# Kernel optimization log

Hardware: AMD Instinct MI355X
Metric: run time of the kernel (lower is better)

## Reference

```python
import jax, jax.numpy as jnp
import numpy as np

N_NODES = 100_000
N_EDGES = 3_200_000
NUM_FEATURES = 128
HIDDEN = 128
NUM_CLASSES = 10
LAYERS = 3
NUM_GRAPHS = 256
EPS = 1e-5


def setup_inputs() -> dict:
    key = jax.random.key(0)
    ks = jax.random.split(key, 12)
    s = 0.05
    x = jax.random.normal(ks[0], (N_NODES, NUM_FEATURES), jnp.float32)
    edge_index = jax.random.randint(ks[1], (2, N_EDGES), 0, N_NODES, dtype=jnp.int32)
    batch = jnp.sort(jax.random.randint(ks[2], (N_NODES,), 0, NUM_GRAPHS, dtype=jnp.int32))
    lin1_W = jax.random.normal(ks[3], (NUM_FEATURES, HIDDEN), jnp.float32) * s
    lin1_b = jnp.zeros((HIDDEN,), jnp.float32)
    conv_W = jax.random.normal(ks[4], (LAYERS, HIDDEN, HIDDEN), jnp.float32) * s
    conv_b = jnp.zeros((LAYERS, HIDDEN), jnp.float32)
    mlp_W1 = jax.random.normal(ks[5], (HIDDEN, HIDDEN), jnp.float32) * s
    mlp_b1 = jnp.zeros((HIDDEN,), jnp.float32)
    mlp_W2 = jax.random.normal(ks[6], (HIDDEN, NUM_CLASSES), jnp.float32) * s
    mlp_b2 = jnp.zeros((NUM_CLASSES,), jnp.float32)
    return {
        'x': x, 'edge_index': edge_index, 'batch': batch,
        'lin1_W': lin1_W, 'lin1_b': lin1_b,
        'conv_W': conv_W, 'conv_b': conv_b,
        'mlp_W1': mlp_W1, 'mlp_b1': mlp_b1,
        'mlp_W2': mlp_W2, 'mlp_b2': mlp_b2,
    }


def reference(x, edge_index, batch, lin1_W, lin1_b, conv_W, conv_b,
              mlp_W1, mlp_b1, mlp_W2, mlp_b2):
    N = x.shape[0]
    # GCN with self-loops, all-ones edge_weight, symmetric normalization.
    loop = jnp.arange(N, dtype=edge_index.dtype)
    src = jnp.concatenate([edge_index[0], loop])
    dst = jnp.concatenate([edge_index[1], loop])
    ew = jnp.ones(src.shape[0], x.dtype)
    deg = jax.ops.segment_sum(ew, dst, num_segments=N)
    dinv = jnp.where(deg > 0, jax.lax.rsqrt(deg), 0.0)
    norm = dinv[src] * dinv[dst]  # [E+N]

    h = jax.nn.relu(x @ lin1_W + lin1_b)  # dropout is identity at eval
    for i in range(conv_W.shape[0]):
        hw = h @ conv_W[i]                       # [N,H]
        msg = hw[src] * norm[:, None]            # [E+N,H] gather
        h = jax.ops.segment_sum(msg, dst, num_segments=N) + conv_b[i]
        h = jax.nn.relu(h)
        # full-tensor LayerNorm (normalized_shape == x.size(), no affine)
        mu = jnp.mean(h)
        var = jnp.mean(jnp.square(h - mu))
        h = (h - mu) * jax.lax.rsqrt(var + EPS)

    # global mean pooling over graphs
    cnt = jax.ops.segment_sum(jnp.ones((N,), x.dtype), batch, num_segments=NUM_GRAPHS)
    pooled = jax.ops.segment_sum(h, batch, num_segments=NUM_GRAPHS) / jnp.maximum(cnt, 1.0)[:, None]

    g = jax.nn.relu(pooled @ mlp_W1 + mlp_b1)
    scores = g @ mlp_W2 + mlp_b2
    return jax.nn.log_softmax(scores, axis=-1)
```

## Files before the change

kernel.cpp:

```cpp
#include <hip/hip_runtime.h>
#include <math.h>

#define NN 100000
#define HH 128
#define NCLS 10
#define NGRAPH 256
#define EPSLN 1e-5f
#define NB 196
#define NBLK 256
#define NREP 8

typedef __attribute__((ext_vector_type(8))) short short8;
typedef __attribute__((ext_vector_type(4))) float f32x4;

static __device__ __forceinline__ unsigned short f2bf(float f){
  unsigned u = __float_as_uint(f);
  u = u + 0x7fffu + ((u >> 16) & 1u);
  return (unsigned short)(u >> 16);
}
static __device__ __forceinline__ float bf2f(unsigned short h){
  return __uint_as_float(((unsigned)h) << 16);
}

__global__ __launch_bounds__(1024) void bucket_hist(
    const int* __restrict__ dst, int E,
    int* __restrict__ gbucket, int* __restrict__ blkbase)
{
  __shared__ int lh[NREP*NB];
  int tid = threadIdx.x;
  for (int i = tid; i < NREP*NB; i += 1024) lh[i] = 0;
  __syncthreads();
  int rep = (tid >> 7) & (NREP-1);
  int* lhr = &lh[rep*NB];
  int per = (E + gridDim.x - 1) / gridDim.x;
  int s = blockIdx.x * per, e = min(E, s + per);
  for (int j = s + tid; j < e; j += 1024)
    atomicAdd(&lhr[dst[j] >> 9], 1);
  __syncthreads();
  for (int i = tid; i < NREP*NB; i += 1024){
    int r = i / NB, bkt = i - r*NB;
    blkbase[((size_t)blockIdx.x*NREP + r)*NB + bkt] = atomicAdd(&gbucket[bkt], lh[i]);
  }
}

__global__ __launch_bounds__(256) void misc_prep(
    const int* __restrict__ gbucket, int* __restrict__ bucket_base, int E,
    int* __restrict__ row_ptr, int N,
    float* __restrict__ params, float* __restrict__ stats, int* __restrict__ counters,
    const float* __restrict__ lin1W, const float* __restrict__ convW,
    unsigned short* __restrict__ WtAll, float* __restrict__ csums)
{
  int b = blockIdx.x;
  if (b == 0){
    if (threadIdx.x == 0){
      int run = 0;
      for (int i = 0; i < NB; i++){ bucket_base[i] = run; run += gbucket[i]; }
      bucket_base[NB] = run;
      row_ptr[N] = E;
      params[0] = 0.f;
      params[1] = 1.f;
      for (int i = 0; i < 6; i++) stats[i] = 0.f;
      for (int i = 0; i < 3; i++) counters[i] = 0;
    }
  } else if (b <= 3){
    int m = b - 1;
    if (threadIdx.x < HH){
      const float* w = convW + (size_t)m*HH*HH;
      float s = 0.f;
      for (int k = 0; k < HH; k++) s += w[k*HH + threadIdx.x];
      csums[m*HH + threadIdx.x] = s;
    }
  } else {
    int m = b - 4;
    const float* srcW = (m == 0) ? lin1W : convW + (size_t)(m-1)*HH*HH;
    unsigned short* dstW = WtAll + (size_t)m*HH*HH;
    for (int i = threadIdx.x; i < HH*HH; i += 256){
      int k = i >> 7, nn2 = i & 127;
      dstW[nn2*HH + k] = f2bf(srcW[i]);
    }
  }
}

__global__ __launch_bounds__(1024) void bucket_scatter(
    const int* __restrict__ src, const int* __restrict__ dst, int E,
    const int* __restrict__ bucket_base, const int* __restrict__ blkbase,
    unsigned* __restrict__ ebuf)
{
  __shared__ int lcur[NREP*NB];
  int tid = threadIdx.x;
  for (int i = tid; i < NREP*NB; i += 1024){
    int r = i / NB, bkt = i - r*NB;
    lcur[i] = bucket_base[bkt] + blkbase[((size_t)blockIdx.x*NREP + r)*NB + bkt];
  }
  __syncthreads();
  int rep = (tid >> 7) & (NREP-1);
  int* lcr = &lcur[rep*NB];
  int per = (E + gridDim.x - 1) / gridDim.x;
  int s = blockIdx.x * per, e = min(E, s + per);
  for (int j = s + tid; j < e; j += 1024){
    int d = dst[j];
    int p = atomicAdd(&lcr[d >> 9], 1);
    ebuf[p] = (((unsigned)(d & 511)) << 23) | (unsigned)src[j];
  }
}

__global__ __launch_bounds__(1024) void bucket_fill(
    const unsigned* __restrict__ ebuf,
    const int* __restrict__ bucket_base, int N,
    int* __restrict__ row_ptr, float* __restrict__ dinv,
    int* __restrict__ csr)
{
  __shared__ int ldeg[512];
  __shared__ int lscan[512];
  __shared__ int lcur[512];
  int b = blockIdx.x, tid = threadIdx.x;
  int node0 = b << 9;
  int nn = min(512, N - node0);
  for (int i = tid; i < 512; i += 1024) ldeg[i] = 0;
  __syncthreads();
  int s = bucket_base[b], e = bucket_base[b + 1];
  for (int j = s + tid; j < e; j += 1024)
    atomicAdd(&ldeg[ebuf[j] >> 23], 1);
  __syncthreads();
  if (tid < 512) lscan[tid] = ldeg[tid];
  __syncthreads();
  for (int off = 1; off < 512; off <<= 1){
    int v = (tid < 512 && tid >= off) ? lscan[tid - off] : 0;
    __syncthreads();
    if (tid < 512) lscan[tid] += v;
    __syncthreads();
  }
  if (tid < nn){
    int rp = s + lscan[tid] - ldeg[tid];
    row_ptr[node0 + tid] = rp;
    lcur[tid] = rp;
    dinv[node0 + tid] = rsqrtf((float)(ldeg[tid] + 1));
  }
  __syncthreads();
  for (int j = s + tid; j < e; j += 1024){
    unsigned pk = ebuf[j];
    int p = atomicAdd(&lcur[pk >> 23], 1);
    csr[p] = (int)(pk & 0x7fffffu);
  }
}

__global__ __launch_bounds__(256) void gemm_mfma(
    const float* __restrict__ A32, const unsigned short* __restrict__ A16,
    const unsigned short* __restrict__ Wt,
    const float* __restrict__ bias, const float* __restrict__ dinv,
    const float* __restrict__ params, const float* __restrict__ colsum,
    unsigned short* __restrict__ out, int n, int mode)
{
  __shared__ unsigned short As[128*128];
  __shared__ unsigned short Ws[128*128];
  int tid = threadIdx.x;
  int rb = blockIdx.x * 128;

  #pragma unroll
  for (int rep = 0; rep < 8; rep++){
    int idx = rep*256 + tid;
    int r = idx >> 4, j = idx & 15;
    uint4 v = *(const uint4*)&Wt[r*HH + j*8];
    *(uint4*)&Ws[r*128 + ((j ^ (r & 7)) << 3)] = v;
  }
  if (mode == 1){
    #pragma unroll
    for (int rep = 0; rep < 8; rep++){
      int idx = rep*256 + tid;
      int r = idx >> 4, j = idx & 15;
      int row = rb + r;
      uint4 v = make_uint4(0,0,0,0);
      if (row < n) v = *(const uint4*)&A16[(size_t)row*HH + j*8];
      *(uint4*)&As[r*128 + ((j ^ (r & 7)) << 3)] = v;
    }
  } else {
    #pragma unroll
    for (int rep = 0; rep < 16; rep++){
      int idx = rep*256 + tid;
      int r = idx >> 5, j4 = idx & 31;
      int row = rb + r;
      float4 v = make_float4(0,0,0,0);
      if (row < n) v = *(const float4*)&A32[(size_t)row*HH + j4*4];
      uint2 pk;
      pk.x = (unsigned)f2bf(v.x) | ((unsigned)f2bf(v.y) << 16);
      pk.y = (unsigned)f2bf(v.z) | ((unsigned)f2bf(v.w) << 16);
      int uidx = r*128 + ((((j4 >> 1) ^ (r & 7)) << 3)) + (j4 & 1)*4;
      *(uint2*)&As[uidx] = pk;
    }
  }
  __syncthreads();

  int l = tid & 63, w = tid >> 6;
  int lr = l & 15, lk = l >> 4;
  f32x4 acc[2][8];
  #pragma unroll
  for (int mt = 0; mt < 2; mt++)
    #pragma unroll
    for (int nt = 0; nt < 8; nt++) acc[mt][nt] = (f32x4)(0.f);

  #pragma unroll
  for (int kc = 0; kc < 4; kc++){
    short8 af[2];
    #pragma unroll
    for (int mt = 0; mt < 2; mt++){
      int row = w*32 + mt*16 + lr;
      af[mt] = *(const short8*)&As[row*128 + (((kc*4 + lk) ^ (row & 7)) << 3)];
    }
    #pragma unroll
    for (int nt = 0; nt < 8; nt++){
      int col = nt*16 + lr;
      short8 bf = *(const short8*)&Ws[col*128 + (((kc*4 + lk) ^ (col & 7)) << 3)];
      acc[0][nt] = __builtin_amdgcn_mfma_f32_16x16x32_bf16(af[0], bf, acc[0][nt], 0, 0, 0);
      acc[1][nt] = __builtin_amdgcn_mfma_f32_16x16x32_bf16(af[1], bf, acc[1][nt], 0, 0, 0);
    }
  }

  float mu = 0.f, rsig = 1.f;
  if (mode == 1){ mu = params[0]; rsig = params[1]; }
  float dvs[2][4];
  #pragma unroll
  for (int mt = 0; mt < 2; mt++)
    #pragma unroll
    for (int r = 0; r < 4; r++){
      int row = rb + w*32 + mt*16 + lk*4 + r;
      dvs[mt][r] = (mode == 1 && row < n) ? dinv[row] : 0.f;
    }
  #pragma unroll
  for (int nt = 0; nt < 8; nt++){
    int col = nt*16 + lr;
    float cs = (mode == 1) ? colsum[col] : 0.f;
    float bb = (mode == 0) ? bias[col] : 0.f;
    #pragma unroll
    for (int mt = 0; mt < 2; mt++){
      #pragma unroll
      for (int r = 0; r < 4; r++){
        int row = rb + w*32 + mt*16 + lk*4 + r;
        if (row < n){
          float a = acc[mt][nt][r];
          float vv = (mode == 0) ? fmaxf(a + bb, 0.f)
                                 : dvs[mt][r] * rsig * (a - mu*cs);
          out[(size_t)row*HH + col] = f2bf(vv);
        }
      }
    }
  }
}

__global__ __launch_bounds__(256) void aggregate(
    const unsigned* __restrict__ hw, const int* __restrict__ row_ptr,
    const int* __restrict__ csr, const float* __restrict__ dinv,
    const float* __restrict__ bias, unsigned* __restrict__ hout,
    float2* __restrict__ partials, int n)
{
  int wid = __builtin_amdgcn_readfirstlane(threadIdx.x >> 6);
  int node = blockIdx.x * 4 + wid;
  if (node >= n) return;
  int l = threadIdx.x & 63;
  int selfoff = node*64 + l;
  unsigned selfv = hw[selfoff];
  float ax = __uint_as_float(selfv << 16);
  float ay = __uint_as_float(selfv & 0xffff0000u);
  int s0 = row_ptr[node], s1 = row_ptr[node+1];
  int j = s0;
  if (j + 16 <= s1){
    int cur[16];
    #pragma unroll
    for (int u = 0; u < 16; u++) cur[u] = csr[j+u];
    while (true){
      unsigned v[16];
      #pragma unroll
      for (int u = 0; u < 16; u++) v[u] = hw[cur[u]*64 + l];
      int jn = j + 16;
      bool more = (jn + 16 <= s1);
      int nxt[16];
      if (more){
        #pragma unroll
        for (int u = 0; u < 16; u++) nxt[u] = csr[jn+u];
      }
      #pragma unroll
      for (int u = 0; u < 16; u++){
        ax += __uint_as_float(v[u] << 16);
        ay += __uint_as_float(v[u] & 0xffff0000u);
      }
      j = jn;
      if (!more) break;
      #pragma unroll
      for (int u = 0; u < 16; u++) cur[u] = nxt[u];
    }
  }
  for (; j + 4 <= s1; j += 4){
    int i0 = csr[j], i1 = csr[j+1], i2 = csr[j+2], i3 = csr[j+3];
    unsigned v0 = hw[i0*64+l], v1 = hw[i1*64+l], v2 = hw[i2*64+l], v3 = hw[i3*64+l];
    ax += (__uint_as_float(v0<<16) + __uint_as_float(v1<<16))
        + (__uint_as_float(v2<<16) + __uint_as_float(v3<<16));
    ay += (__uint_as_float(v0&0xffff0000u) + __uint_as_float(v1&0xffff0000u))
        + (__uint_as_float(v2&0xffff0000u) + __uint_as_float(v3&0xffff0000u));
  }
  for (; j < s1; j++){
    unsigned v = hw[csr[j]*64 + l];
    ax += __uint_as_float(v << 16);
    ay += __uint_as_float(v & 0xffff0000u);
  }
  float dv = dinv[node];
  float2 bb = ((const float2*)bias)[l];
  float rx = fmaxf(fmaf(dv, ax, bb.x), 0.f);
  float ry = fmaxf(fmaf(dv, ay, bb.y), 0.f);
  hout[selfoff] = (unsigned)f2bf(rx) | ((unsigned)f2bf(ry) << 16);

  float s = rx + ry, q = rx*rx + ry*ry;
  #pragma unroll
  for (int off = 32; off > 0; off >>= 1){
    s += __shfl_xor(s, off, 64);
    q += __shfl_xor(q, off, 64);
  }
  if (l == 0) partials[node] = make_float2(s, q);
}

__global__ __launch_bounds__(256) void finalize_ln(
    const float2* __restrict__ partials, int n, float* __restrict__ stats,
    int* __restrict__ counter, float* __restrict__ params)
{
  int tid = threadIdx.x;
  float s = 0.f, q = 0.f;
  for (int i = blockIdx.x*256 + tid; i < n; i += gridDim.x*256){
    float2 p = partials[i];
    s += p.x; q += p.y;
  }
  #pragma unroll
  for (int off = 32; off > 0; off >>= 1){
    s += __shfl_xor(s, off, 64);
    q += __shfl_xor(q, off, 64);
  }
  __shared__ float ssm[4], qsm[4];
  int wave = tid >> 6, lane = tid & 63;
  if (lane == 0){ ssm[wave] = s; qsm[wave] = q; }
  __syncthreads();
  if (tid == 0){
    atomicAdd(&stats[0], ssm[0]+ssm[1]+ssm[2]+ssm[3]);
    atomicAdd(&stats[1], qsm[0]+qsm[1]+qsm[2]+qsm[3]);
    __threadfence();
    int done = atomicAdd(counter, 1);
    if (done == (int)gridDim.x - 1){
      float S = atomicAdd(&stats[0], 0.f);
      float Q = atomicAdd(&stats[1], 0.f);
      const float inv = 1.f / ((float)NN * (float)HH);
      float mu = S * inv;
      float var = Q * inv - mu*mu;
      params[0] = mu;
      params[1] = rsqrtf(var + EPSLN);
    }
  }
}

__global__ __launch_bounds__(128) void pool_mlp(
    const unsigned short* __restrict__ h, const int* __restrict__ batch,
    const float* __restrict__ params, const float* __restrict__ W1,
    const float* __restrict__ b1, const float* __restrict__ W2,
    const float* __restrict__ b2, float* __restrict__ out, int n)
{
  __shared__ float pooled[128];
  __shared__ float gact[128];
  __shared__ float sc[16];
  __shared__ int se[2];
  int g = blockIdx.x, tid = threadIdx.x;
  if (tid < 2){
    int v = g + tid;
    int lo = 0, hi = n;
    while (lo < hi){ int mid = (lo+hi) >> 1; if (batch[mid] < v) lo = mid+1; else hi = mid; }
    se[tid] = lo;
  }
  __syncthreads();
  int start = se[0], end = se[1];
  float sum = 0.f;
  for (int v = start; v < end; v++) sum += bf2f(h[(size_t)v*HH + tid]);
  float cnt = (float)((end - start) > 0 ? (end - start) : 1);
  float mu = params[0], rs = params[1];
  pooled[tid] = rs * (sum / cnt - mu);
  __syncthreads();
  float a = b1[tid];
  for (int k = 0; k < HH; k++) a = fmaf(pooled[k], W1[k*HH + tid], a);
  gact[tid] = fmaxf(a, 0.f);
  __syncthreads();
  if (tid < NCLS){
    float s = b2[tid];
    for (int k = 0; k < HH; k++) s = fmaf(gact[k], W2[k*NCLS + tid], s);
    sc[tid] = s;
  }
  __syncthreads();
  if (tid == 0){
    float m = sc[0];
    for (int j = 1; j < NCLS; j++) m = fmaxf(m, sc[j]);
    float lse = 0.f;
    for (int j = 0; j < NCLS; j++) lse += expf(sc[j] - m);
    lse = logf(lse);
    for (int j = 0; j < NCLS; j++) out[g*NCLS + j] = sc[j] - m - lse;
  }
}

extern "C" void kernel_launch(void* const* d_in, const int* in_sizes, int n_in,
                              void* d_out, int out_size, void* d_ws, size_t ws_size,
                              hipStream_t stream)
{
  const float* x      = (const float*)d_in[0];
  const int*   ei     = (const int*)d_in[1];
  const int*   batch  = (const int*)d_in[2];
  const float* lin1_W = (const float*)d_in[3];
  const float* lin1_b = (const float*)d_in[4];
  const float* conv_W = (const float*)d_in[5];
  const float* conv_b = (const float*)d_in[6];
  const float* mlp_W1 = (const float*)d_in[7];
  const float* mlp_b1 = (const float*)d_in[8];
  const float* mlp_W2 = (const float*)d_in[9];
  const float* mlp_b2 = (const float*)d_in[10];

  const int N = in_sizes[2];
  const int E = in_sizes[1] / 2;

  char* ws = (char*)d_ws;
  size_t off = 0;
  auto alloc = [&](size_t bytes)->char*{
    char* p = ws + off; off += (bytes + 255) & ~(size_t)255; return p;
  };
  unsigned short* bufA = (unsigned short*)alloc((size_t)N*HH*2);
  unsigned short* bufB = (unsigned short*)alloc((size_t)N*HH*2);
  unsigned short* WtAll= (unsigned short*)alloc((size_t)4*HH*HH*2);
  int*      csr     = (int*)     alloc((size_t)E*4);
  unsigned* ebuf    = (unsigned*)alloc((size_t)E*4);
  int*      row_ptr = (int*)     alloc((size_t)(N+1)*4);
  float*    dinv    = (float*)   alloc((size_t)N*4);
  int*      gbucket = (int*)     alloc((size_t)NB*4);
  int*      bucket_base = (int*) alloc((size_t)(NB+1)*4);
  int*      blkbase = (int*)     alloc((size_t)NBLK*NREP*NB*4);
  float*    params  = (float*)   alloc(256);
  float*    stats   = (float*)   alloc(256);
  int*      counters= (int*)     alloc(256);
  float*    csums   = (float*)   alloc(3*HH*4);
  float2*   partials= (float2*)  alloc((size_t)N*8);

  const int* srcp = ei;
  const int* dstp = ei + E;

  hipMemsetAsync(gbucket, 0, (size_t)NB*4, stream);
  bucket_hist<<<NBLK, 1024, 0, stream>>>(dstp, E, gbucket, blkbase);
  misc_prep<<<8, 256, 0, stream>>>(gbucket, bucket_base, E, row_ptr, N,
                                   params, stats, counters,
                                   lin1_W, conv_W, WtAll, csums);
  bucket_scatter<<<NBLK, 1024, 0, stream>>>(srcp, dstp, E, bucket_base, blkbase, ebuf);
  bucket_fill<<<NB, 1024, 0, stream>>>(ebuf, bucket_base, N, row_ptr, dinv, csr);

  int gblocks = (N + 127) / 128;
  gemm_mfma<<<gblocks, 256, 0, stream>>>(x, nullptr, WtAll, lin1_b,
                                         nullptr, nullptr, nullptr, bufA, N, 0);
  for (int i = 0; i < 3; i++){
    gemm_mfma<<<gblocks, 256, 0, stream>>>(nullptr, bufA, WtAll + (size_t)(i+1)*HH*HH,
                                           nullptr, dinv, params + 2*i, csums + i*HH,
                                           bufB, N, 1);
    aggregate<<<(N+3)/4, 256, 0, stream>>>((const unsigned*)bufB, row_ptr, csr, dinv,
                                           conv_b + i*HH, (unsigned*)bufA, partials, N);
    finalize_ln<<<64, 256, 0, stream>>>(partials, N, stats + 2*i,
                                        counters + i, params + 2*(i+1));
  }
  pool_mlp<<<NGRAPH, 128, 0, stream>>>(bufA, batch, params + 6,
                                       mlp_W1, mlp_b1, mlp_W2, mlp_b2,
                                       (float*)d_out, N);
}
```

Baseline: 679.5 us.

## Split aggregation across feature halves and parallelize pooling over nodes

The aggregate kernel now launches a 2D grid in which each block handles half of the feature columns. Each wave splits into two 32-lane halves that gather alternate neighbors, and the two halves are combined with a cross-lane shuffle. This gives more independent 128-byte gathers per wave and doubles the block count, in exchange for reading each CSR index twice and writing twice as many LN partials. The pool_mlp kernel moves to 1024 threads: 16 waves sum node rows in parallel, and W1 is staged in shared memory, which removes the serial per-graph loop over nodes.

```diff
diff --git a/kernel.cpp b/kernel.cpp
--- a/kernel.cpp
+++ b/kernel.cpp
@@ -255,74 +255,74 @@
   int wid = __builtin_amdgcn_readfirstlane(threadIdx.x >> 6);
   int node = blockIdx.x * 4 + wid;
   if (node >= n) return;
+  int half = blockIdx.y;
   int l = threadIdx.x & 63;
-  int selfoff = node*64 + l;
-  unsigned selfv = hw[selfoff];
-  float ax = __uint_as_float(selfv << 16);
-  float ay = __uint_as_float(selfv & 0xffff0000u);
+  int sub = l >> 5;
+  int f = l & 31;
+  int base = half*32 + f;
+
+  float ax = 0.f, ay = 0.f;
+  if (sub == 0){
+    unsigned sv = hw[node*64 + base];
+    ax = __uint_as_float(sv << 16);
+    ay = __uint_as_float(sv & 0xffff0000u);
+  }
   int s0 = row_ptr[node], s1 = row_ptr[node+1];
   int j = s0;
-  if (j + 16 <= s1){
-    int cur[16];
-    #pragma unroll
-    for (int u = 0; u < 16; u++) cur[u] = csr[j+u];
-    while (true){
-      unsigned v[16];
-      #pragma unroll
-      for (int u = 0; u < 16; u++) v[u] = hw[cur[u]*64 + l];
-      int jn = j + 16;
-      bool more = (jn + 16 <= s1);
-      int nxt[16];
-      if (more){
-        #pragma unroll
-        for (int u = 0; u < 16; u++) nxt[u] = csr[jn+u];
-      }
-      #pragma unroll
-      for (int u = 0; u < 16; u++){
-        ax += __uint_as_float(v[u] << 16);
-        ay += __uint_as_float(v[u] & 0xffff0000u);
-      }
-      j = jn;
-      if (!more) break;
-      #pragma unroll
-      for (int u = 0; u < 16; u++) cur[u] = nxt[u];
-    }
-  }
-  for (; j + 4 <= s1; j += 4){
-    int i0 = csr[j], i1 = csr[j+1], i2 = csr[j+2], i3 = csr[j+3];
-    unsigned v0 = hw[i0*64+l], v1 = hw[i1*64+l], v2 = hw[i2*64+l], v3 = hw[i3*64+l];
-    ax += (__uint_as_float(v0<<16) + __uint_as_float(v1<<16))
-        + (__uint_as_float(v2<<16) + __uint_as_float(v3<<16));
-    ay += (__uint_as_float(v0&0xffff0000u) + __uint_as_float(v1&0xffff0000u))
-        + (__uint_as_float(v2&0xffff0000u) + __uint_as_float(v3&0xffff0000u));
-  }
-  for (; j < s1; j++){
-    unsigned v = hw[csr[j]*64 + l];
+  for (; j + 16 <= s1; j += 16){
+    int idx[8];
+    #pragma unroll
+    for (int u = 0; u < 8; u++){
+      int a0 = csr[j + 2*u];
+      int a1 = csr[j + 2*u + 1];
+      idx[u] = sub ? a1 : a0;
+    }
+    unsigned v[8];
+    #pragma unroll
+    for (int u = 0; u < 8; u++) v[u] = hw[idx[u]*64 + base];
+    #pragma unroll
+    for (int u = 0; u < 8; u++){
+      ax += __uint_as_float(v[u] << 16);
+      ay += __uint_as_float(v[u] & 0xffff0000u);
+    }
+  }
+  for (; j + 2 <= s1; j += 2){
+    int a0 = csr[j], a1 = csr[j + 1];
+    unsigned v = hw[(sub ? a1 : a0)*64 + base];
     ax += __uint_as_float(v << 16);
     ay += __uint_as_float(v & 0xffff0000u);
   }
+  if (j < s1 && sub == 0){
+    unsigned v = hw[csr[j]*64 + base];
+    ax += __uint_as_float(v << 16);
+    ay += __uint_as_float(v & 0xffff0000u);
+  }
+  ax += __shfl_xor(ax, 32, 64);
+  ay += __shfl_xor(ay, 32, 64);
+
   float dv = dinv[node];
-  float2 bb = ((const float2*)bias)[l];
+  float2 bb = ((const float2*)bias)[base];
   float rx = fmaxf(fmaf(dv, ax, bb.x), 0.f);
   float ry = fmaxf(fmaf(dv, ay, bb.y), 0.f);
-  hout[selfoff] = (unsigned)f2bf(rx) | ((unsigned)f2bf(ry) << 16);
+  if (sub == 0)
+    hout[node*64 + base] = (unsigned)f2bf(rx) | ((unsigned)f2bf(ry) << 16);
 
   float s = rx + ry, q = rx*rx + ry*ry;
   #pragma unroll
-  for (int off = 32; off > 0; off >>= 1){
+  for (int off = 16; off > 0; off >>= 1){
     s += __shfl_xor(s, off, 64);
     q += __shfl_xor(q, off, 64);
   }
-  if (l == 0) partials[node] = make_float2(s, q);
+  if (l == 0) partials[node*2 + half] = make_float2(s, q);
 }
 
 __global__ __launch_bounds__(256) void finalize_ln(
-    const float2* __restrict__ partials, int n, float* __restrict__ stats,
+    const float2* __restrict__ partials, int n2, float* __restrict__ stats,
     int* __restrict__ counter, float* __restrict__ params)
 {
   int tid = threadIdx.x;
   float s = 0.f, q = 0.f;
-  for (int i = blockIdx.x*256 + tid; i < n; i += gridDim.x*256){
+  for (int i = blockIdx.x*256 + tid; i < n2; i += gridDim.x*256){
     float2 p = partials[i];
     s += p.x; q += p.y;
   }
@@ -352,17 +352,25 @@
   }
 }
 
-__global__ __launch_bounds__(128) void pool_mlp(
-    const unsigned short* __restrict__ h, const int* __restrict__ batch,
+__global__ __launch_bounds__(1024) void pool_mlp(
+    const unsigned* __restrict__ h, const int* __restrict__ batch,
     const float* __restrict__ params, const float* __restrict__ W1,
     const float* __restrict__ b1, const float* __restrict__ W2,
     const float* __restrict__ b2, float* __restrict__ out, int n)
 {
+  __shared__ float W1s[128*128];
+  __shared__ float2 psum[16][64];
   __shared__ float pooled[128];
   __shared__ float gact[128];
   __shared__ float sc[16];
   __shared__ int se[2];
   int g = blockIdx.x, tid = threadIdx.x;
+
+  #pragma unroll
+  for (int rep = 0; rep < 4; rep++){
+    int i = rep*1024 + tid;
+    *(float4*)&W1s[i*4] = *(const float4*)&W1[i*4];
+  }
   if (tid < 2){
     int v = g + tid;
     int lo = 0, hi = n;
@@ -371,15 +379,33 @@
   }
   __syncthreads();
   int start = se[0], end = se[1];
-  float sum = 0.f;
-  for (int v = start; v < end; v++) sum += bf2f(h[(size_t)v*HH + tid]);
-  float cnt = (float)((end - start) > 0 ? (end - start) : 1);
-  float mu = params[0], rs = params[1];
-  pooled[tid] = rs * (sum / cnt - mu);
-  __syncthreads();
-  float a = b1[tid];
-  for (int k = 0; k < HH; k++) a = fmaf(pooled[k], W1[k*HH + tid], a);
-  gact[tid] = fmaxf(a, 0.f);
+  int w = tid >> 6, l = tid & 63;
+  float sx = 0.f, sy = 0.f;
+  for (int v = start + w; v < end; v += 16){
+    unsigned u = h[v*64 + l];
+    sx += __uint_as_float(u << 16);
+    sy += __uint_as_float(u & 0xffff0000u);
+  }
+  psum[w][l] = make_float2(sx, sy);
+  __syncthreads();
+  if (tid < 64){
+    float ax = 0.f, ay = 0.f;
+    #pragma unroll
+    for (int ww = 0; ww < 16; ww++){
+      float2 p = psum[ww][tid];
+      ax += p.x; ay += p.y;
+    }
+    float cnt = (float)((end - start) > 0 ? (end - start) : 1);
+    float mu = params[0], rs = params[1];
+    pooled[tid*2]   = rs * (ax / cnt - mu);
+    pooled[tid*2+1] = rs * (ay / cnt - mu);
+  }
+  __syncthreads();
+  if (tid < 128){
+    float a = b1[tid];
+    for (int k = 0; k < HH; k++) a = fmaf(pooled[k], W1s[k*HH + tid], a);
+    gact[tid] = fmaxf(a, 0.f);
+  }
   __syncthreads();
   if (tid < NCLS){
     float s = b2[tid];
@@ -435,7 +461,7 @@
   float*    stats   = (float*)   alloc(256);
   int*      counters= (int*)     alloc(256);
   float*    csums   = (float*)   alloc(3*HH*4);
-  float2*   partials= (float2*)  alloc((size_t)N*8);
+  float2*   partials= (float2*)  alloc((size_t)N*2*8);
 
   const int* srcp = ei;
   const int* dstp = ei + E;
@@ -451,16 +477,17 @@
   int gblocks = (N + 127) / 128;
   gemm_mfma<<<gblocks, 256, 0, stream>>>(x, nullptr, WtAll, lin1_b,
                                          nullptr, nullptr, nullptr, bufA, N, 0);
+  dim3 agrid((N + 3) / 4, 2);
   for (int i = 0; i < 3; i++){
     gemm_mfma<<<gblocks, 256, 0, stream>>>(nullptr, bufA, WtAll + (size_t)(i+1)*HH*HH,
                                            nullptr, dinv, params + 2*i, csums + i*HH,
                                            bufB, N, 1);
-    aggregate<<<(N+3)/4, 256, 0, stream>>>((const unsigned*)bufB, row_ptr, csr, dinv,
-                                           conv_b + i*HH, (unsigned*)bufA, partials, N);
-    finalize_ln<<<64, 256, 0, stream>>>(partials, N, stats + 2*i,
+    aggregate<<<agrid, 256, 0, stream>>>((const unsigned*)bufB, row_ptr, csr, dinv,
+                                         conv_b + i*HH, (unsigned*)bufA, partials, N);
+    finalize_ln<<<64, 256, 0, stream>>>(partials, 2*N, stats + 2*i,
                                         counters + i, params + 2*(i+1));
   }
-  pool_mlp<<<NGRAPH, 128, 0, stream>>>(bufA, batch, params + 6,
-                                       mlp_W1, mlp_b1, mlp_W2, mlp_b2,
-                                       (float*)d_out, N);
-}
+  pool_mlp<<<NGRAPH, 1024, 0, stream>>>((const unsigned*)bufA, batch, params + 6,
+                                        mlp_W1, mlp_b1, mlp_W2, mlp_b2,
+                                        (float*)d_out, N);
+}
```

Result: faster. 649.2 us (-4.5%).
